# Kernel tuning notes

Hardware: AMD Instinct MI355X
Metric: run time of the kernel (lower is better)

The kernel has to match this reference:

```python
import jax, jax.numpy as jnp
import numpy as np

T_SCALE = 160
NUM_SAMPLE = 32
FEAT_DIM = 2048
HIDDEN = 512
N_CLASS = 20
BATCH = 8


def build_sample_mask(tscale=T_SCALE, ns=NUM_SAMPLE):
    # Vectorized version of _get_interp1d_mask (prop_boundary_ratio=0, num_sample_perbin=1).
    # Returns mask of shape [tscale, ns, start, end] (already transposed as in the torch code).
    s = np.arange(tscale)[:, None, None]           # start
    e = np.arange(tscale)[None, :, None]           # end
    k = np.arange(ns)[None, None, :]
    pos = s + (e - s) * k / (ns - 1.0)             # [T, T, ns] sample positions
    Sg, Eg, Kg = np.broadcast_arrays(s, e, k)
    posf = pos.ravel(); Sf = Sg.ravel(); Ef = Eg.ravel(); Kf = Kg.ravel()
    valid = Ef >= Sf
    frac, dn = np.modf(posf)
    dn = dn.astype(np.int64)
    up = np.ceil(posf).astype(np.int64)
    mask = np.zeros((tscale, ns, tscale, tscale), dtype=np.float32)
    m1 = valid & (dn >= 0) & (dn <= tscale - 1)
    np.add.at(mask, (dn[m1], Kf[m1], Sf[m1], Ef[m1]), (1.0 - frac[m1]).astype(np.float32))
    m2 = valid & (up >= 0) & (up <= tscale - 1)
    np.add.at(mask, (up[m2], Kf[m2], Sf[m2], Ef[m2]), frac[m2].astype(np.float32))
    return jnp.asarray(mask)


def conv1d(x, w, padding):
    # x: [B, Cin, T], w: [Cout, Cin, K]
    return jax.lax.conv_general_dilated(
        x, w, window_strides=(1,), padding=[(padding, padding)],
        dimension_numbers=("NCH", "OIH", "NCH"))


def setup_inputs() -> dict:
    key = jax.random.key(0)
    ks = jax.random.split(key, 6)
    x = jax.random.normal(ks[0], (BATCH, T_SCALE, FEAT_DIM), dtype=jnp.float32)
    w1 = jax.random.normal(ks[1], (HIDDEN, FEAT_DIM, 3), dtype=jnp.float32) * 0.02
    b1 = jnp.zeros((HIDDEN,), dtype=jnp.float32)
    wc = jax.random.normal(ks[2], (N_CLASS, HIDDEN, 1), dtype=jnp.float32) * 0.05
    wa = jax.random.normal(ks[3], (1, HIDDEN, 3), dtype=jnp.float32) * 0.05
    ba = jnp.zeros((1,), dtype=jnp.float32)
    sample_mask = build_sample_mask()  # [T, ns, T, T]
    return {"x": x, "sample_mask": sample_mask, "w1": w1, "b1": b1,
            "wc": wc, "wa": wa, "ba": ba}


def reference(x, sample_mask, w1, b1, wc, wa, ba):
    ns = NUM_SAMPLE
    q = ns // 4  # 8
    xp = jnp.transpose(x, (0, 2, 1))                   # [B, F, T]
    feat = jax.nn.relu(conv1d(xp, w1, 1) + b1[None, :, None])   # [B, H, T] (dropout = eval/identity)
    y_class = conv1d(feat, wc, 0)                      # [B, C, T]
    y_atn = conv1d(feat, wa, 1) + ba[None, :, None]    # [B, 1, T]
    # boundary matching: matmul against sparse interpolation mask
    out = jnp.einsum("bct,tkij->bckij", y_class, sample_mask)   # [B, C, ns, T, T]
    out_start = out[:, :, :q].mean(axis=2)
    out_mid = out[:, :, q:ns - q].mean(axis=2)
    out_end = out[:, :, ns - q:].mean(axis=2)
    bmn_class = jnp.concatenate((out_start, out_mid, out_end), axis=1)  # [B, 3C, T, T]
    sig = jax.nn.sigmoid(y_atn)
    x_fg = (sig * feat).sum(-1, keepdims=True) / (sig.sum(-1, keepdims=True) + 1e-8)  # [B, H, 1]
    y_fg = jnp.einsum("oh,bht->bot", wc[:, :, 0], x_fg)  # conv_class 1x1, no bias
    return (y_class, y_fg, bmn_class)
```

## Files before the change

kernel.cpp:

```cpp
#include <hip/hip_runtime.h>
#include <math.h>

#define TS 160
#define FEATD 2048
#define HID 512
#define NC 20
#define NB 8

typedef __attribute__((ext_vector_type(8))) short bfrag;
typedef __attribute__((ext_vector_type(4))) float f32x4;

static __device__ __forceinline__ unsigned short f2bf(float f) {
  unsigned int u = __float_as_uint(f);
  unsigned int r = (u + 0x7FFFu + ((u >> 16) & 1u)) >> 16;
  return (unsigned short)r;
}

static __device__ __forceinline__ void gload16(const void* g, void* l) {
  __builtin_amdgcn_global_load_lds((const __attribute__((address_space(1))) void*)g,
                                   (__attribute__((address_space(3))) void*)l, 16, 0, 0);
}

__global__ __launch_bounds__(256) void k_cvt(const float* __restrict__ x,
                                             const float* __restrict__ w1,
                                             unsigned short* __restrict__ xb,
                                             unsigned short* __restrict__ wb) {
  __shared__ float Ls[FEATD * 3];
  const int tid = threadIdx.x;
  if (blockIdx.x < 1296) {
    const int idx = blockIdx.x * 256 + tid;
    const int c = (idx & 255) * 8;
    const int row = idx >> 8;
    const int b = row / 162, pr = row - b * 162;
    unsigned short* o = xb + (size_t)row * FEATD + c;
    if (pr == 0 || pr == 161) {
      *(uint4*)o = make_uint4(0u, 0u, 0u, 0u);
    } else {
      const float* src = x + ((size_t)(b * TS + pr - 1)) * FEATD + c;
      float4 v0 = *(const float4*)src;
      float4 v1 = *(const float4*)(src + 4);
      unsigned short r[8] = {f2bf(v0.x), f2bf(v0.y), f2bf(v0.z), f2bf(v0.w),
                             f2bf(v1.x), f2bf(v1.y), f2bf(v1.z), f2bf(v1.w)};
      *(uint4*)o = *(const uint4*)r;
    }
  } else {
    const int h = blockIdx.x - 1296;
    const float4* src = (const float4*)(w1 + (size_t)h * (FEATD * 3));
    for (int e = tid; e < FEATD * 3 / 4; e += 256) ((float4*)Ls)[e] = src[e];
    __syncthreads();
    for (int oc = tid; oc < 768; oc += 256) {
      const int tap = oc >> 8;
      const int f0 = (oc & 255) * 8;
      unsigned short r[8];
      #pragma unroll
      for (int i = 0; i < 8; ++i) r[i] = f2bf(Ls[(f0 + i) * 3 + tap]);
      *(uint4*)&wb[((size_t)tap * HID + h) * FEATD + f0] = *(const uint4*)r;
    }
  }
}

__global__ __launch_bounds__(256, 2) void k_conv_mfma(const unsigned short* __restrict__ xb,
                                                      const unsigned short* __restrict__ wb,
                                                      float* __restrict__ part) {
  const int bb = blockIdx.x;
  const int h0 = blockIdx.y * 64;
  const int kz = blockIdx.z;
  const int tid = threadIdx.x;
  const int wid = tid >> 6, lane = tid & 63;

  __shared__ unsigned short Alds[162 * 64];
  __shared__ unsigned short Blds[3 * 64 * 64];

  const unsigned short* xbb = xb + (size_t)bb * 162 * FEATD;
  const unsigned short* wbb = wb + (size_t)h0 * FEATD;

  f32x4 acc[5][2] = {};
  const int wr = wid >> 1, wc = wid & 1;

  for (int s = 0; s < 4; ++s) {
    const int f0 = kz * 256 + s * 64;
    #pragma unroll
    for (int is = 0; is < 5; ++is) {
      const int ci = is * 256 + wid * 64 + lane;
      const int row = ci >> 3, c = ci & 7;
      gload16(xbb + (size_t)row * FEATD + f0 + ((c ^ (row & 7)) << 3),
              (char*)Alds + (size_t)(is * 256 + wid * 64) * 16);
    }
    #pragma unroll
    for (int is = 0; is < 6; ++is) {
      const int ci = is * 256 + wid * 64 + lane;
      const int tap = ci >> 9, rr = (ci >> 3) & 63, c = ci & 7;
      gload16(wbb + (size_t)tap * (HID * FEATD) + (size_t)rr * FEATD + f0 + ((c ^ (rr & 7)) << 3),
              (char*)Blds + (size_t)(is * 256 + wid * 64) * 16);
    }
    if (tid < 16) {
      const int row = 160 + (tid >> 3), c = tid & 7;
      uint4 v = *(const uint4*)(xbb + (size_t)row * FEATD + f0 + ((c ^ (row & 7)) << 3));
      *(uint4*)((char*)Alds + row * 128 + c * 16) = v;
    }
    __syncthreads();

    #pragma unroll
    for (int tap = 0; tap < 3; ++tap) {
      #pragma unroll
      for (int kk = 0; kk < 2; ++kk) {
        const int cread = kk * 4 + (lane >> 4);
        bfrag bf0, bf1;
        {
          const int hh0 = wc * 32 + (lane & 15);
          const int hh1 = hh0 + 16;
          bf0 = *(const bfrag*)((char*)Blds + tap * 8192 + hh0 * 128 + ((cread ^ (hh0 & 7)) << 4));
          bf1 = *(const bfrag*)((char*)Blds + tap * 8192 + hh1 * 128 + ((cread ^ (hh1 & 7)) << 4));
        }
        #pragma unroll
        for (int mi = 0; mi < 5; ++mi) {
          const int rr = wr * 80 + mi * 16 + (lane & 15) + tap;
          bfrag af = *(const bfrag*)((char*)Alds + rr * 128 + ((cread ^ (rr & 7)) << 4));
          acc[mi][0] = __builtin_amdgcn_mfma_f32_16x16x32_bf16(af, bf0, acc[mi][0], 0, 0, 0);
          acc[mi][1] = __builtin_amdgcn_mfma_f32_16x16x32_bf16(af, bf1, acc[mi][1], 0, 0, 0);
        }
      }
    }
    __syncthreads();
  }

  float* pout = part + (size_t)kz * (NB * TS) * HID;
  #pragma unroll
  for (int mi = 0; mi < 5; ++mi) {
    const int r0 = bb * TS + wr * 80 + mi * 16 + (lane >> 4) * 4;
    #pragma unroll
    for (int ni = 0; ni < 2; ++ni) {
      const int c0 = h0 + wc * 32 + ni * 16 + (lane & 15);
      #pragma unroll
      for (int i = 0; i < 4; ++i)
        pout[(size_t)(r0 + i) * HID + c0] = acc[mi][ni][i];
    }
  }
}

__global__ __launch_bounds__(256) void k_bias_relu(const float* __restrict__ part,
                                                   const float* __restrict__ bias,
                                                   float* __restrict__ feat) {
  const int idx = blockIdx.x * 256 + threadIdx.x;
  const float4* p = (const float4*)part;
  float4 a = p[idx];
  #pragma unroll
  for (int k = 1; k < 8; ++k) {
    float4 v = p[(size_t)k * 163840 + idx];
    a.x += v.x; a.y += v.y; a.z += v.z; a.w += v.w;
  }
  const float4 bb = ((const float4*)bias)[idx & 127];
  float4 o;
  o.x = fmaxf(a.x + bb.x, 0.f);
  o.y = fmaxf(a.y + bb.y, 0.f);
  o.z = fmaxf(a.z + bb.z, 0.f);
  o.w = fmaxf(a.w + bb.w, 0.f);
  ((float4*)feat)[idx] = o;
}

__global__ __launch_bounds__(256) void k_head(const float* __restrict__ feat,
                                              const float* __restrict__ wc,
                                              const float* __restrict__ wa,
                                              const float* __restrict__ ba,
                                              float* __restrict__ y_class,
                                              float* __restrict__ y_atn) {
  __shared__ float wcs[NC * HID];
  __shared__ float was[HID * 3];
  const int tid = threadIdx.x;
  for (int e = tid; e < NC * HID; e += 256) wcs[e] = wc[e];
  for (int e = tid; e < HID * 3; e += 256) was[e] = wa[e];
  __syncthreads();
  const int wave = blockIdx.x * 4 + (tid >> 6);
  const int lane = tid & 63;
  const int b = wave / TS, t = wave - b * TS;
  const float* frow = &feat[((size_t)b * TS + t) * HID];
  float fc[8], fm[8], fp[8];
  #pragma unroll
  for (int i2 = 0; i2 < 8; ++i2) {
    int h = lane + 64 * i2;
    fc[i2] = frow[h];
    fm[i2] = (t > 0)      ? frow[h - HID] : 0.f;
    fp[i2] = (t < TS - 1) ? frow[h + HID] : 0.f;
  }
  #pragma unroll 4
  for (int c = 0; c < NC; ++c) {
    float p = 0.f;
    #pragma unroll
    for (int i2 = 0; i2 < 8; ++i2) p += fc[i2] * wcs[c * HID + lane + 64 * i2];
    #pragma unroll
    for (int off = 32; off; off >>= 1) p += __shfl_xor(p, off);
    if (lane == 0) y_class[((size_t)b * NC + c) * TS + t] = p;
  }
  float p = 0.f;
  #pragma unroll
  for (int i2 = 0; i2 < 8; ++i2) {
    int h = lane + 64 * i2;
    p += fm[i2] * was[h * 3 + 0] + fc[i2] * was[h * 3 + 1] + fp[i2] * was[h * 3 + 2];
  }
  #pragma unroll
  for (int off = 32; off; off >>= 1) p += __shfl_xor(p, off);
  if (lane == 0) y_atn[b * TS + t] = p + ba[0];
}

__global__ __launch_bounds__(256) void k_fg(const float* __restrict__ feat,
                                            const float* __restrict__ y_atn,
                                            const float* __restrict__ wc,
                                            float* __restrict__ y_fg) {
  const int b = blockIdx.x;
  const int tid = threadIdx.x;
  __shared__ float sig[TS];
  __shared__ float red[4];
  __shared__ float xfg[HID];
  float s = 0.f;
  if (tid < TS) { s = 1.f / (1.f + expf(-y_atn[b * TS + tid])); sig[tid] = s; }
  float r = s;
  #pragma unroll
  for (int off = 32; off; off >>= 1) r += __shfl_xor(r, off);
  if ((tid & 63) == 0) red[tid >> 6] = r;
  __syncthreads();
  const float inv = 1.f / (red[0] + red[1] + red[2] + red[3] + 1e-8f);
  for (int h = tid; h < HID; h += 256) {
    float a = 0.f;
    for (int t = 0; t < TS; ++t) a += sig[t] * feat[((size_t)b * TS + t) * HID + h];
    xfg[h] = a * inv;
  }
  __syncthreads();
  const int wv = tid >> 6, lane = tid & 63;
  for (int c = wv; c < NC; c += 4) {
    float p = 0.f;
    #pragma unroll
    for (int i2 = 0; i2 < 8; ++i2) {
      int h = lane + 64 * i2;
      p += wc[c * HID + h] * xfg[h];
    }
    #pragma unroll
    for (int off = 32; off; off >>= 1) p += __shfl_xor(p, off);
    if (lane == 0) y_fg[b * NC + c] = p;
  }
}

__global__ __launch_bounds__(256) void k_bmn(const float* __restrict__ y_class,
                                             float* __restrict__ bmn) {
  const int b = blockIdx.x / 100;
  const int blk = blockIdx.x - b * 100;
  const int tid = threadIdx.x;
  __shared__ float Ys[TS * 32];
  for (int e = tid; e < NC * TS; e += 256) {
    int c = e / TS, t = e - c * TS;
    Ys[t * 32 + (((c >> 2) ^ (t & 7)) << 2) + (c & 3)] = y_class[((size_t)b * NC + c) * TS + t];
  }
  __syncthreads();
  const int idx = blk * 256 + tid;
  const int i = idx / TS, j = idx - i * TS;
  float* ob = bmn + (size_t)b * 60 * TS * TS + (size_t)i * TS + j;
  const size_t cs = (size_t)TS * TS;
  if (j < i) {
    #pragma unroll 4
    for (int gc = 0; gc < 60; ++gc) ob[(size_t)gc * cs] = 0.f;
    return;
  }
  float ac[NC];
  auto step = [&](int k) {
    float pos = (float)(k * (j - i)) / 31.0f + (float)i;
    int dn = (int)pos;
    float frx = pos - (float)dn;
    int up = dn + (frx > 0.f ? 1 : 0);
    float wd = 1.f - frx;
    const float* yd = &Ys[dn * 32];
    const float* yu = &Ys[up * 32];
    #pragma unroll
    for (int c4 = 0; c4 < 5; ++c4) {
      float4 d4 = *(const float4*)(yd + ((c4 ^ (dn & 7)) << 2));
      float4 u4 = *(const float4*)(yu + ((c4 ^ (up & 7)) << 2));
      ac[c4 * 4 + 0] += wd * d4.x + frx * u4.x;
      ac[c4 * 4 + 1] += wd * d4.y + frx * u4.y;
      ac[c4 * 4 + 2] += wd * d4.z + frx * u4.z;
      ac[c4 * 4 + 3] += wd * d4.w + frx * u4.w;
    }
  };
  #pragma unroll
  for (int c = 0; c < NC; ++c) ac[c] = 0.f;
  #pragma unroll 2
  for (int k = 0; k < 8; ++k) step(k);
  #pragma unroll
  for (int c = 0; c < NC; ++c) ob[(size_t)c * cs] = ac[c] * 0.125f;
  #pragma unroll
  for (int c = 0; c < NC; ++c) ac[c] = 0.f;
  #pragma unroll 2
  for (int k = 8; k < 24; ++k) step(k);
  #pragma unroll
  for (int c = 0; c < NC; ++c) ob[(size_t)(NC + c) * cs] = ac[c] * 0.0625f;
  #pragma unroll
  for (int c = 0; c < NC; ++c) ac[c] = 0.f;
  #pragma unroll 2
  for (int k = 24; k < 32; ++k) step(k);
  #pragma unroll
  for (int c = 0; c < NC; ++c) ob[(size_t)(2 * NC + c) * cs] = ac[c] * 0.125f;
}

extern "C" void kernel_launch(void* const* d_in, const int* in_sizes, int n_in,
                              void* d_out, int out_size, void* d_ws, size_t ws_size,
                              hipStream_t stream) {
  const float* x  = (const float*)d_in[0];
  const float* w1 = (const float*)d_in[2];
  const float* b1 = (const float*)d_in[3];
  const float* wc = (const float*)d_in[4];
  const float* wa = (const float*)d_in[5];
  const float* ba = (const float*)d_in[6];

  float* out     = (float*)d_out;
  float* y_class = out;
  float* y_fg    = out + NB * NC * TS;
  float* bmn     = out + NB * NC * TS + NB * NC;

  float* part  = (float*)d_ws;
  float* feat  = part + 8 * NB * TS * HID;
  float* y_atn = feat + NB * TS * HID;
  unsigned short* xb = (unsigned short*)(y_atn + 2048);
  unsigned short* wb = xb + (size_t)NB * 162 * FEATD;

  k_cvt<<<1296 + 512, 256, 0, stream>>>(x, w1, xb, wb);
  k_conv_mfma<<<dim3(8, 8, 8), 256, 0, stream>>>(xb, wb, part);
  k_bias_relu<<<640, 256, 0, stream>>>(part, b1, feat);
  k_head<<<320, 256, 0, stream>>>(feat, wc, wa, ba, y_class, y_atn);
  k_fg<<<8, 256, 0, stream>>>(feat, y_atn, wc, y_fg);
  k_bmn<<<800, 256, 0, stream>>>(y_class, bmn);
}
```

Measured before the change: 85.85 us.

## Recast boundary-matching interpolation as bf16 MFMA GEMM with precomputed weight table

```diff
diff --git a/kernel.cpp b/kernel.cpp
--- a/kernel.cpp
+++ b/kernel.cpp
@@ -59,7 +59,27 @@
   }
 }
 
-__global__ __launch_bounds__(256, 2) void k_conv_mfma(const unsigned short* __restrict__ xb,
+__global__ __launch_bounds__(256) void k_wbuild(unsigned short* __restrict__ WT) {
+  const int idx = blockIdx.x * 256 + threadIdx.x;
+  const int tau = idx % 160;
+  const int dd = (idx / 160) % 320;
+  const int g = idx / (160 * 320);
+  float w = 0.f;
+  if (dd >= 160) {
+    const int d = dd - 160;
+    const int k0 = (g == 0) ? 0 : (g == 1 ? 8 : 24);
+    const int k1 = (g == 0) ? 8 : (g == 1 ? 24 : 32);
+    for (int k = k0; k < k1; ++k) {
+      float p = (float)(d * k) / 31.0f;
+      float a = fabsf(p - (float)tau);
+      w += fmaxf(0.f, 1.f - a);
+    }
+    w *= (g == 1) ? 0.0625f : 0.125f;
+  }
+  WT[idx] = f2bf(w);
+}
+
+__global__ __launch_bounds__(256, 3) void k_conv_mfma(const unsigned short* __restrict__ xb,
                                                       const unsigned short* __restrict__ wb,
                                                       float* __restrict__ part) {
   const int bb = blockIdx.x;
@@ -239,63 +259,84 @@
   }
 }
 
-__global__ __launch_bounds__(256) void k_bmn(const float* __restrict__ y_class,
-                                             float* __restrict__ bmn) {
-  const int b = blockIdx.x / 100;
-  const int blk = blockIdx.x - b * 100;
-  const int tid = threadIdx.x;
-  __shared__ float Ys[TS * 32];
-  for (int e = tid; e < NC * TS; e += 256) {
-    int c = e / TS, t = e - c * TS;
-    Ys[t * 32 + (((c >> 2) ^ (t & 7)) << 2) + (c & 3)] = y_class[((size_t)b * NC + c) * TS + t];
+__global__ __launch_bounds__(256) void k_ysbuild(const float* __restrict__ y_class,
+                                                 unsigned short* __restrict__ Ys) {
+  const int idx = blockIdx.x * 256 + threadIdx.x;
+  const int c8 = idx % 42;
+  const int bc = (idx / 42) % 160;
+  const int s = idx / (42 * 160);
+  unsigned short r[8];
+  #pragma unroll
+  for (int e = 0; e < 8; ++e) {
+    const int tpos = c8 * 8 + e + s;
+    r[e] = (c8 * 8 + e < 336 && tpos < 160) ? f2bf(y_class[bc * 160 + tpos]) : (unsigned short)0;
+  }
+  *(uint4*)&Ys[((size_t)s * 160 + bc) * 336 + c8 * 8] = *(const uint4*)r;
+}
+
+__global__ __launch_bounds__(256, 1) void k_bmn_mfma(const unsigned short* __restrict__ Ys,
+                                                     const unsigned short* __restrict__ WT,
+                                                     float* __restrict__ bmn) {
+  const int i = blockIdx.x;
+  const int g = blockIdx.y;
+  const int tid = threadIdx.x;
+  const int wid = tid >> 6, lane = tid & 63;
+
+  __shared__ char Alds[65536];
+  __shared__ char Wlds[65536];
+
+  const int s = i & 7;
+  const char* ysb = (const char*)(Ys + (size_t)s * 160 * 336) + (size_t)(i - s) * 2;
+  const char* wtb = (const char*)(WT + (size_t)g * 320 * 160) + (size_t)(160 - i) * 320;
+
+  #pragma unroll
+  for (int it = 0; it < 16; ++it) {
+    const int idx = it * 256 + tid;
+    int row = idx / 25, c = idx - row * 25;
+    if (row > 159) row = 159;
+    if (c > 19) c = 0;
+    gload16(ysb + (size_t)row * 672 + c * 16, Alds + (size_t)idx * 16);
+    gload16(wtb + (size_t)row * 320 + c * 16, Wlds + (size_t)idx * 16);
   }
   __syncthreads();
-  const int idx = blk * 256 + tid;
-  const int i = idx / TS, j = idx - i * TS;
-  float* ob = bmn + (size_t)b * 60 * TS * TS + (size_t)i * TS + j;
-  const size_t cs = (size_t)TS * TS;
-  if (j < i) {
-    #pragma unroll 4
-    for (int gc = 0; gc < 60; ++gc) ob[(size_t)gc * cs] = 0.f;
-    return;
-  }
-  float ac[NC];
-  auto step = [&](int k) {
-    float pos = (float)(k * (j - i)) / 31.0f + (float)i;
-    int dn = (int)pos;
-    float frx = pos - (float)dn;
-    int up = dn + (frx > 0.f ? 1 : 0);
-    float wd = 1.f - frx;
-    const float* yd = &Ys[dn * 32];
-    const float* yu = &Ys[up * 32];
-    #pragma unroll
-    for (int c4 = 0; c4 < 5; ++c4) {
-      float4 d4 = *(const float4*)(yd + ((c4 ^ (dn & 7)) << 2));
-      float4 u4 = *(const float4*)(yu + ((c4 ^ (up & 7)) << 2));
-      ac[c4 * 4 + 0] += wd * d4.x + frx * u4.x;
-      ac[c4 * 4 + 1] += wd * d4.y + frx * u4.y;
-      ac[c4 * 4 + 2] += wd * d4.z + frx * u4.z;
-      ac[c4 * 4 + 3] += wd * d4.w + frx * u4.w;
-    }
-  };
-  #pragma unroll
-  for (int c = 0; c < NC; ++c) ac[c] = 0.f;
-  #pragma unroll 2
-  for (int k = 0; k < 8; ++k) step(k);
-  #pragma unroll
-  for (int c = 0; c < NC; ++c) ob[(size_t)c * cs] = ac[c] * 0.125f;
-  #pragma unroll
-  for (int c = 0; c < NC; ++c) ac[c] = 0.f;
-  #pragma unroll 2
-  for (int k = 8; k < 24; ++k) step(k);
-  #pragma unroll
-  for (int c = 0; c < NC; ++c) ob[(size_t)(NC + c) * cs] = ac[c] * 0.0625f;
-  #pragma unroll
-  for (int c = 0; c < NC; ++c) ac[c] = 0.f;
-  #pragma unroll 2
-  for (int k = 24; k < 32; ++k) step(k);
-  #pragma unroll
-  for (int c = 0; c < NC; ++c) ob[(size_t)(2 * NC + c) * cs] = ac[c] * 0.125f;
+
+  const int wr = wid >> 1, wc = wid & 1;
+  f32x4 acc[5][5] = {};
+
+  #pragma unroll
+  for (int ks = 0; ks < 5; ++ks) {
+    const int cc = ks * 4 + (lane >> 4);
+    bfrag bfr[5];
+    #pragma unroll
+    for (int nf = 0; nf < 5; ++nf) {
+      const int j = wc * 80 + nf * 16 + (lane & 15);
+      bfr[nf] = *(const bfrag*)(Wlds + (size_t)j * 400 + cc * 16);
+    }
+    #pragma unroll
+    for (int mf = 0; mf < 5; ++mf) {
+      const int r = wr * 80 + mf * 16 + (lane & 15);
+      bfrag af = *(const bfrag*)(Alds + (size_t)r * 400 + cc * 16);
+      #pragma unroll
+      for (int nf = 0; nf < 5; ++nf)
+        acc[mf][nf] = __builtin_amdgcn_mfma_f32_16x16x32_bf16(af, bfr[nf], acc[mf][nf], 0, 0, 0);
+    }
+  }
+
+  #pragma unroll
+  for (int mf = 0; mf < 5; ++mf) {
+    const int r0 = wr * 80 + mf * 16 + (lane >> 4) * 4;
+    #pragma unroll
+    for (int reg = 0; reg < 4; ++reg) {
+      const int r = r0 + reg;
+      const int b = r / 20, c = r - b * 20;
+      float* base = bmn + (((size_t)(b * 60 + g * 20 + c) * TS) + i) * TS;
+      #pragma unroll
+      for (int nf = 0; nf < 5; ++nf) {
+        const int j = wc * 80 + nf * 16 + (lane & 15);
+        base[j] = acc[mf][nf][reg];
+      }
+    }
+  }
 }
 
 extern "C" void kernel_launch(void* const* d_in, const int* in_sizes, int n_in,
@@ -318,11 +359,15 @@
   float* y_atn = feat + NB * TS * HID;
   unsigned short* xb = (unsigned short*)(y_atn + 2048);
   unsigned short* wb = xb + (size_t)NB * 162 * FEATD;
-
+  unsigned short* WT = wb + (size_t)3 * HID * FEATD;
+  unsigned short* Ys = WT + (size_t)3 * 320 * 160;
+
+  k_wbuild<<<600, 256, 0, stream>>>(WT);
   k_cvt<<<1296 + 512, 256, 0, stream>>>(x, w1, xb, wb);
   k_conv_mfma<<<dim3(8, 8, 8), 256, 0, stream>>>(xb, wb, part);
   k_bias_relu<<<640, 256, 0, stream>>>(part, b1, feat);
   k_head<<<320, 256, 0, stream>>>(feat, wc, wa, ba, y_class, y_atn);
   k_fg<<<8, 256, 0, stream>>>(feat, y_atn, wc, y_fg);
-  k_bmn<<<800, 256, 0, stream>>>(y_class, bmn);
-}
+  k_ysbuild<<<210, 256, 0, stream>>>(y_class, Ys);
+  k_bmn_mfma<<<dim3(160, 3), 256, 0, stream>>>(Ys, WT, bmn);
+}
```

Result: faster. 80.73 us (-6.0%).
